# Optimization experiments

Hardware: AMD Instinct MI355X
Metric: run time of the kernel (lower is better)

## Reference

```python
import jax, jax.numpy as jnp
import numpy as np

NUM_HEADS = 8
NUM_GROUPS = 32  # min(C//4, 32) for C=512
EPS = 1e-6       # flax GroupNorm default


def setup_inputs() -> dict:
    key = jax.random.key(0)
    ks = jax.random.split(key, 3)
    B, H, W, D, C = 2, 16, 16, 16, 512
    x = jax.random.normal(ks[0], (B, H, W, D, C), dtype=jnp.float32)
    w_qkv = jax.random.normal(ks[1], (C, 3 * C), dtype=jnp.float32) / np.sqrt(C)
    w_proj = jax.random.normal(ks[2], (C, C), dtype=jnp.float32) / np.sqrt(C)
    return {
        "x": x,
        "gn_scale": jnp.ones((C,), jnp.float32),
        "gn_bias": jnp.zeros((C,), jnp.float32),
        "w_qkv": w_qkv,
        "b_qkv": jnp.zeros((3 * C,), jnp.float32),
        "w_proj": w_proj,
        "b_proj": jnp.zeros((C,), jnp.float32),
    }


def group_norm(x, scale, bias):
    # x: [B, S, C]; normalize within each of NUM_GROUPS channel groups over (S, group-channels)
    B, S, C = x.shape
    xg = x.reshape(B, S, NUM_GROUPS, C // NUM_GROUPS)
    mean = jnp.mean(xg, axis=(1, 3), keepdims=True)
    var = jnp.var(xg, axis=(1, 3), keepdims=True)
    xn = (xg - mean) * jax.lax.rsqrt(var + EPS)
    return xn.reshape(B, S, C) * scale + bias


def reference(x, gn_scale, gn_bias, w_qkv, b_qkv, w_proj, b_proj):
    B, H, W, D, C = x.shape
    S = H * W * D
    hd = C // NUM_HEADS
    xf = x.reshape(B, S, C)
    q_in = group_norm(xf, gn_scale, gn_bias)
    # 1x1x1 conv == per-position dense
    qkv = q_in @ w_qkv + b_qkv                      # [B, S, 3C]
    qkv = qkv.reshape(B, S, NUM_HEADS, 3 * hd)
    q, k, v = jnp.split(qkv, 3, axis=-1)            # each [B, S, nh, hd]
    scale = 1.0 / jnp.sqrt(jnp.asarray(hd, x.dtype))
    logits = jnp.einsum('btnh,bfnh->bnft', k, q * scale)  # [B, nh, S, S]
    weights = jax.nn.softmax(logits, axis=-1)
    h = jnp.einsum('bnft,btnh->bfnh', weights, v)   # [B, S, nh, hd]
    h = h.reshape(B, S, C) @ w_proj + b_proj
    return h.reshape(x.shape) + x
```

## Files before the change

kernel.cpp:

```cpp
#include <hip/hip_runtime.h>

typedef __attribute__((ext_vector_type(8))) short short8;
typedef __attribute__((ext_vector_type(4))) float f32x4;
typedef __attribute__((ext_vector_type(16))) float f32x16;

#define S_LEN 4096
#define C_DIM 512
#define NH 8
#define HD 64
#define NG 32
#define GS 16
#define LOG2E 1.44269504088896340736f

__device__ __forceinline__ unsigned short f2bf(float f) {
  union { float f; unsigned int u; } v; v.f = f;
  unsigned int r = v.u + 0x7fffu + ((v.u >> 16) & 1u);
  return (unsigned short)(r >> 16);
}

__device__ __forceinline__ float bf2f(unsigned short s) {
  union { unsigned u; float f; } v; v.u = (unsigned)s << 16;
  return v.f;
}

__device__ __forceinline__ float fexp2(float x) {
  float r;
  asm("v_exp_f32 %0, %1" : "=v"(r) : "v"(x));
  return r;
}

__device__ __forceinline__ unsigned pk_bf16(float a, float b) {
  unsigned r;
  asm("v_cvt_pk_bf16_f32 %0, %1, %2" : "=v"(r) : "v"(a), "v"(b));
  return r;
}

__device__ __forceinline__ void pl_swap(unsigned& a, unsigned& b) {
  asm("v_permlane32_swap_b32 %0, %1" : "+v"(a), "+v"(b));
}
__device__ __forceinline__ void pl_swapf(float& a, float& b) {
  asm("v_permlane32_swap_b32 %0, %1" : "+v"(a), "+v"(b));
}

__device__ __forceinline__ void gload_lds16(const void* g, void* l) {
  __builtin_amdgcn_global_load_lds((const __attribute__((address_space(1))) void*)g,
                                   (__attribute__((address_space(3))) void*)l, 16, 0, 0);
}

__global__ __launch_bounds__(256) void prep_kernel(const float* __restrict__ x,
                                                   float* __restrict__ partials,
                                                   const float* __restrict__ w_qkv,
                                                   unsigned short* __restrict__ wqkvT,
                                                   const float* __restrict__ w_proj,
                                                   unsigned short* __restrict__ wprojT) {
  __shared__ float tile[32][33];
  __shared__ float r1[4], r2[4];
  int bid = blockIdx.x;
  if (bid < 256) {
    int bg = bid >> 2, chunk = bid & 3;
    int b = bg >> 5, g = bg & 31;
    const float* xp = x + (size_t)b * S_LEN * C_DIM + g * GS;
    float s1 = 0.f, s2 = 0.f;
    for (int i = threadIdx.x; i < 1024 * 4; i += 256) {
      int s = chunk * 1024 + (i >> 2), c4 = i & 3;
      float4 v = *(const float4*)&xp[(size_t)s * C_DIM + c4 * 4];
      s1 += v.x + v.y + v.z + v.w;
      s2 += v.x * v.x + v.y * v.y + v.z * v.z + v.w * v.w;
    }
    for (int off = 1; off < 64; off <<= 1) {
      s1 += __shfl_xor(s1, off);
      s2 += __shfl_xor(s2, off);
    }
    int w = threadIdx.x >> 6;
    if ((threadIdx.x & 63) == 0) { r1[w] = s1; r2[w] = s2; }
    __syncthreads();
    if (threadIdx.x == 0) {
      partials[bg * 8 + chunk * 2]     = r1[0] + r1[1] + r1[2] + r1[3];
      partials[bg * 8 + chunk * 2 + 1] = r2[0] + r2[1] + r2[2] + r2[3];
    }
    return;
  }
  const float* src; unsigned short* dst; int K, N, n0, k0;
  if (bid < 1024) {
    int t = bid - 256;  src = w_qkv;  dst = wqkvT;  K = 512; N = 1536;
    n0 = (t % 48) * 32; k0 = (t / 48) * 32;
  } else {
    int t = bid - 1024; src = w_proj; dst = wprojT; K = 512; N = 512;
    n0 = (t % 16) * 32; k0 = (t / 16) * 32;
  }
  int c = threadIdx.x & 31, r0 = threadIdx.x >> 5;
  for (int i = 0; i < 4; ++i) {
    int r = r0 + i * 8;
    tile[r][c] = src[(size_t)(k0 + r) * N + n0 + c];
  }
  __syncthreads();
  for (int i = 0; i < 4; ++i) {
    int r = r0 + i * 8;
    dst[(size_t)(n0 + r) * K + k0 + c] = f2bf(tile[c][r]);
  }
}

__global__ __launch_bounds__(256) void gemm_qkv_kernel(const float* __restrict__ x,
                                                       const float* __restrict__ partials,
                                                       const float* __restrict__ gscale,
                                                       const float* __restrict__ gbias,
                                                       const unsigned short* __restrict__ Bt,
                                                       const float* __restrict__ qbias,
                                                       unsigned short* __restrict__ qh,
                                                       unsigned short* __restrict__ kh,
                                                       unsigned short* __restrict__ vh) {
  __shared__ unsigned char Alds[16384];
  __shared__ unsigned char Blds[16384];
  __shared__ float AsL[512], CsL[512];
  int tid = threadIdx.x, lane = tid & 63, w = tid >> 6;
  int li = lane & 15, g = lane >> 4;
  int wr = (w >> 1) * 64, wc = (w & 1) * 64;
  int m0 = blockIdx.y * 128, n0 = blockIdx.x * 128;
  int b_ = m0 >> 12;

  int srow = tid >> 3;
  int colS = (tid & 7) * 16;
  int sc   = colS ^ ((srow & 7) << 4);
  const char* bSrc = (const char*)Bt + (size_t)(n0 + srow) * 1024 + sc;

  const float invN = 1.0f / (float)(S_LEN * GS);
#pragma unroll
  for (int i = 0; i < 2; ++i) {
    int c = tid + i * 256;
    int bg = b_ * NG + (c >> 4);
    float s1 = partials[bg * 8] + partials[bg * 8 + 2] + partials[bg * 8 + 4] + partials[bg * 8 + 6];
    float s2 = partials[bg * 8 + 1] + partials[bg * 8 + 3] + partials[bg * 8 + 5] + partials[bg * 8 + 7];
    float mean = s1 * invN;
    float var = s2 * invN - mean * mean;
    float rstd = rsqrtf(var + 1e-6f);
    float A_ = rstd * gscale[c];
    AsL[c] = A_;
    CsL[c] = gbias[c] - mean * A_;
  }
  __syncthreads();

  int tr = tid >> 1, hf2 = tid & 1;
  const float* xRow = x + (size_t)(m0 + tr) * C_DIM + hf2 * 32;

  f32x4 acc[4][4];
  for (int i = 0; i < 4; ++i)
    for (int j = 0; j < 4; ++j) acc[i][j] = (f32x4){0.f, 0.f, 0.f, 0.f};

  for (int k0 = 0; k0 < 512; k0 += 64) {
    float4 xv[8];
#pragma unroll
    for (int q = 0; q < 8; ++q) xv[q] = *(const float4*)&xRow[k0 + q * 4];
#pragma unroll
    for (int r = 0; r < 4; ++r)
      gload_lds16(bSrc + (size_t)r * 32 * 1024 + k0 * 2, &Blds[r * 4096 + tid * 16]);

    int cbase = k0 + hf2 * 32;
#pragma unroll
    for (int q = 0; q < 4; ++q) {
      union { unsigned u[4]; short8 v; } d;
#pragma unroll
      for (int p = 0; p < 2; ++p) {
        int c = cbase + q * 8 + p * 4;
        float4 A4 = *(const float4*)&AsL[c];
        float4 C4 = *(const float4*)&CsL[c];
        float4 vv = xv[2 * q + p];
        d.u[p * 2]     = pk_bf16(vv.x * A4.x + C4.x, vv.y * A4.y + C4.y);
        d.u[p * 2 + 1] = pk_bf16(vv.z * A4.z + C4.z, vv.w * A4.w + C4.w);
      }
      int cc = hf2 * 64 + q * 16;
      *(short8*)&Alds[tr * 128 + (cc ^ ((tr & 7) << 4))] = d.v;
    }
    __syncthreads();

#pragma unroll
    for (int ks = 0; ks < 2; ++ks) {
      short8 af[4], bfm[4];
#pragma unroll
      for (int mi = 0; mi < 4; ++mi) {
        int row = wr + mi * 16 + li;
        af[mi] = *(const short8*)&Alds[row * 128 + ((ks * 64 + g * 16) ^ ((row & 7) << 4))];
      }
#pragma unroll
      for (int ni = 0; ni < 4; ++ni) {
        int row = wc + ni * 16 + li;
        bfm[ni] = *(const short8*)&Blds[row * 128 + ((ks * 64 + g * 16) ^ ((row & 7) << 4))];
      }
#pragma unroll
      for (int mi = 0; mi < 4; ++mi)
#pragma unroll
        for (int ni = 0; ni < 4; ++ni)
          acc[mi][ni] = __builtin_amdgcn_mfma_f32_16x16x32_bf16(af[mi], bfm[ni], acc[mi][ni], 0, 0, 0);
    }
    __syncthreads();
  }

  for (int ni = 0; ni < 4; ++ni) {
    int n = n0 + wc + ni * 16 + li;
    float bn = qbias[n];
    int head = n / 192;
    int rem = n - head * 192;
    int part = rem >> 6;
    int h = rem & 63;
    if (part == 2) {
      for (int mi = 0; mi < 4; ++mi) {
        int m = m0 + wr + mi * 16 + g * 4;
        int b = m >> 12, s = m & 4095;
        size_t idx = ((size_t)(b * NH + head) * HD + h) * S_LEN + s;
        ushort4 val;
        val.x = f2bf(acc[mi][ni][0] + bn);
        val.y = f2bf(acc[mi][ni][1] + bn);
        val.z = f2bf(acc[mi][ni][2] + bn);
        val.w = f2bf(acc[mi][ni][3] + bn);
        *(ushort4*)&vh[idx] = val;
      }
    } else {
      unsigned short* dst = part == 0 ? qh : kh;
      float mul = part == 0 ? 0.125f * LOG2E : 1.0f;
      for (int mi = 0; mi < 4; ++mi)
        for (int j = 0; j < 4; ++j) {
          int m = m0 + wr + mi * 16 + g * 4 + j;
          int b = m >> 12, s = m & 4095;
          dst[((size_t)(b * NH + head) * S_LEN + s) * HD + h] = f2bf((acc[mi][ni][j] + bn) * mul);
        }
    }
  }
}

__global__ __launch_bounds__(256) void gemm_plain_kernel(const unsigned short* __restrict__ A,
                                                         const unsigned short* __restrict__ Bt,
                                                         const float* __restrict__ bias,
                                                         const float* __restrict__ resid,
                                                         float* __restrict__ outf) {
  __shared__ unsigned char Alds[16384];
  __shared__ unsigned char Blds[16384];
  int tid = threadIdx.x, lane = tid & 63, w = tid >> 6;
  int li = lane & 15, g = lane >> 4;
  int wr = (w >> 1) * 64, wc = (w & 1) * 64;
  int m0 = blockIdx.y * 128, n0 = blockIdx.x * 128;

  int srow = tid >> 3;
  int colS = (tid & 7) * 16;
  int sc   = colS ^ ((srow & 7) << 4);
  const char* aSrc = (const char*)A + (size_t)(m0 + srow) * 1024 + sc;
  const char* bSrc = (const char*)Bt + (size_t)(n0 + srow) * 1024 + sc;

  f32x4 acc[4][4];
  for (int i = 0; i < 4; ++i)
    for (int j = 0; j < 4; ++j) acc[i][j] = (f32x4){0.f, 0.f, 0.f, 0.f};

  for (int k0 = 0; k0 < 512; k0 += 64) {
#pragma unroll
    for (int r = 0; r < 4; ++r) {
      gload_lds16(aSrc + (size_t)r * 32 * 1024 + k0 * 2, &Alds[r * 4096 + tid * 16]);
      gload_lds16(bSrc + (size_t)r * 32 * 1024 + k0 * 2, &Blds[r * 4096 + tid * 16]);
    }
    asm volatile("s_waitcnt vmcnt(0)" ::: "memory");
    __builtin_amdgcn_s_barrier();
#pragma unroll
    for (int ks = 0; ks < 2; ++ks) {
      short8 af[4], bfm[4];
#pragma unroll
      for (int mi = 0; mi < 4; ++mi) {
        int row = wr + mi * 16 + li;
        af[mi] = *(const short8*)&Alds[row * 128 + ((ks * 64 + g * 16) ^ ((row & 7) << 4))];
      }
#pragma unroll
      for (int ni = 0; ni < 4; ++ni) {
        int row = wc + ni * 16 + li;
        bfm[ni] = *(const short8*)&Blds[row * 128 + ((ks * 64 + g * 16) ^ ((row & 7) << 4))];
      }
#pragma unroll
      for (int mi = 0; mi < 4; ++mi)
#pragma unroll
        for (int ni = 0; ni < 4; ++ni)
          acc[mi][ni] = __builtin_amdgcn_mfma_f32_16x16x32_bf16(af[mi], bfm[ni], acc[mi][ni], 0, 0, 0);
    }
    __syncthreads();
  }

  for (int ni = 0; ni < 4; ++ni) {
    int n = n0 + wc + ni * 16 + li;
    float bn = bias[n];
    for (int mi = 0; mi < 4; ++mi)
      for (int j = 0; j < 4; ++j) {
        int m = m0 + wr + mi * 16 + g * 4 + j;
        size_t off = (size_t)m * C_DIM + n;
        outf[off] = acc[mi][ni][j] + bn + resid[off];
      }
  }
}

__global__ __launch_bounds__(256) void gemm_proj_kernel(const unsigned short* __restrict__ opart,
                                                        const float* __restrict__ lpart,
                                                        const unsigned short* __restrict__ Bt,
                                                        const float* __restrict__ bias,
                                                        const float* __restrict__ resid,
                                                        float* __restrict__ outf) {
  __shared__ unsigned char Alds[16384];
  __shared__ unsigned char Blds[16384];
  __shared__ float linv[8][128];
  int tid = threadIdx.x, lane = tid & 63, w = tid >> 6;
  int li = lane & 15, g = lane >> 4;
  int wr = (w >> 1) * 64, wc = (w & 1) * 64;
  int m0 = blockIdx.y * 128, n0 = blockIdx.x * 128;
  int b_ = m0 >> 12;
  int s0 = m0 & 4095;

  int srow = tid >> 3;
  int colS = (tid & 7) * 16;
  int sc   = colS ^ ((srow & 7) << 4);
  const char* bSrc = (const char*)Bt + (size_t)(n0 + srow) * 1024 + sc;

#pragma unroll
  for (int i = 0; i < 4; ++i) {
    int e = tid + i * 256;
    int hd_ = e >> 7, r = e & 127;
    size_t rowA = (size_t)((b_ * NH + hd_) * 2) * S_LEN + s0 + r;
    linv[hd_][r] = 1.0f / (lpart[rowA] + lpart[rowA + S_LEN]);
  }
  __syncthreads();

  int tr = tid >> 1, hf2 = tid & 1;
  size_t rowBase = ((size_t)(b_ * NH) * 2) * S_LEN + s0 + tr;

  f32x4 acc[4][4];
  for (int i = 0; i < 4; ++i)
    for (int j = 0; j < 4; ++j) acc[i][j] = (f32x4){0.f, 0.f, 0.f, 0.f};

  for (int k0 = 0; k0 < 512; k0 += 64) {
    int head = k0 >> 6;
#pragma unroll
    for (int r = 0; r < 4; ++r)
      gload_lds16(bSrc + (size_t)r * 32 * 1024 + k0 * 2, &Blds[r * 4096 + tid * 16]);

    size_t rowA = rowBase + (size_t)head * 2 * S_LEN;
    const unsigned short* pA0 = opart + rowA * 64 + hf2 * 32;
    const unsigned short* pA1 = opart + (rowA + S_LEN) * 64 + hf2 * 32;
    float inv = linv[head][tr];
#pragma unroll
    for (int q = 0; q < 4; ++q) {
      short8 xx = *(const short8*)&pA0[q * 8];
      short8 yy = *(const short8*)&pA1[q * 8];
      union { unsigned u[4]; short8 v; } d;
#pragma unroll
      for (int p = 0; p < 4; ++p) {
        float f0 = (bf2f((unsigned short)xx[2 * p])     + bf2f((unsigned short)yy[2 * p]))     * inv;
        float f1 = (bf2f((unsigned short)xx[2 * p + 1]) + bf2f((unsigned short)yy[2 * p + 1])) * inv;
        d.u[p] = pk_bf16(f0, f1);
      }
      int cc = hf2 * 64 + q * 16;
      *(short8*)&Alds[tr * 128 + (cc ^ ((tr & 7) << 4))] = d.v;
    }
    __syncthreads();

#pragma unroll
    for (int ks = 0; ks < 2; ++ks) {
      short8 af[4], bfm[4];
#pragma unroll
      for (int mi = 0; mi < 4; ++mi) {
        int row = wr + mi * 16 + li;
        af[mi] = *(const short8*)&Alds[row * 128 + ((ks * 64 + g * 16) ^ ((row & 7) << 4))];
      }
#pragma unroll
      for (int ni = 0; ni < 4; ++ni) {
        int row = wc + ni * 16 + li;
        bfm[ni] = *(const short8*)&Blds[row * 128 + ((ks * 64 + g * 16) ^ ((row & 7) << 4))];
      }
#pragma unroll
      for (int mi = 0; mi < 4; ++mi)
#pragma unroll
        for (int ni = 0; ni < 4; ++ni)
          acc[mi][ni] = __builtin_amdgcn_mfma_f32_16x16x32_bf16(af[mi], bfm[ni], acc[mi][ni], 0, 0, 0);
    }
    __syncthreads();
  }

  for (int ni = 0; ni < 4; ++ni) {
    int n = n0 + wc + ni * 16 + li;
    float bn = bias[n];
    for (int mi = 0; mi < 4; ++mi)
      for (int j = 0; j < 4; ++j) {
        int m = m0 + wr + mi * 16 + g * 4 + j;
        size_t off = (size_t)m * C_DIM + n;
        outf[off] = acc[mi][ni][j] + bn + resid[off];
      }
  }
}

template <int SPLIT>
__global__ __launch_bounds__(256, 4) void attn_kernel(const unsigned short* __restrict__ qh,
                                                      const unsigned short* __restrict__ kh,
                                                      const unsigned short* __restrict__ vt,
                                                      unsigned short* __restrict__ ob,
                                                      unsigned short* __restrict__ opart,
                                                      float* __restrict__ lpart) {
  __shared__ unsigned char Kt[3 * 4096];
  __shared__ unsigned char Vt[3 * 4096];
  int bn = blockIdx.y;
  int half = SPLIT > 1 ? blockIdx.z : 0;
  int tid = threadIdx.x, lane = tid & 63, wv = tid >> 6;
  int r32 = lane & 31, hi_ = lane >> 5;
  int q0 = blockIdx.x * 128 + wv * 32;
  const int NT = S_LEN / 32 / SPLIT;
  const unsigned short* qp = qh + (size_t)bn * S_LEN * HD;
  const char* kp = (const char*)(kh + (size_t)bn * S_LEN * HD);
  const char* vp = (const char*)(vt + (size_t)bn * HD * S_LEN);

  int srow  = wv * 8 + (lane >> 3);
  int scolS = (lane & 7) * 16;
  int sc    = scolS ^ ((srow & 7) << 4);
  const char* kSrc = kp + (size_t)srow * 128 + sc + (size_t)half * (S_LEN / SPLIT) * 128;
  int vh_ = srow + ((sc >> 6) << 5);
  const char* vSrc = vp + (size_t)vh_ * (S_LEN * 2) + (sc & 63) + (size_t)half * (S_LEN / SPLIT) * 2;

  short8 qf[4];
#pragma unroll
  for (int ks = 0; ks < 4; ++ks)
    qf[ks] = *(const short8*)&qp[(size_t)(q0 + r32) * HD + ks * 16 + hi_ * 8];

  f32x16 o0, o1, z16;
#pragma unroll
  for (int i = 0; i < 16; ++i) { o0[i] = 0.f; o1[i] = 0.f; z16[i] = 0.f; }
  float lsum = 0.f;

  int swzr = (r32 & 7) << 4;
  int sBase = wv * 1024;

  gload_lds16(kSrc, &Kt[sBase]);
  gload_lds16(vSrc, &Vt[sBase]);
  gload_lds16(kSrc + 32 * 128, &Kt[4096 + sBase]);
  gload_lds16(vSrc + 32 * 2,   &Vt[4096 + sBase]);
  asm volatile("s_waitcnt vmcnt(2)" ::: "memory");
  __builtin_amdgcn_s_barrier();

  int curO = 0, nxtO = 4096, nnO = 8192;
  for (int it = 0; it < NT; ++it) {
    bool more = (it + 2 < NT);
    if (more) {
      size_t t0n = (size_t)(it + 2) * 32;
      gload_lds16(kSrc + t0n * 128, &Kt[nnO + sBase]);
      gload_lds16(vSrc + t0n * 2,   &Vt[nnO + sBase]);
    }

    const unsigned char* Kr = &Kt[curO + r32 * 128];
    const unsigned char* Vr = &Vt[curO + r32 * 128];
    short8 kf[4], vf[4];
#pragma unroll
    for (int ks = 0; ks < 4; ++ks)
      kf[ks] = *(const short8*)&Kr[(ks * 32 + hi_ * 16) ^ swzr];
#pragma unroll
    for (int kk = 0; kk < 2; ++kk)
#pragma unroll
      for (int hf = 0; hf < 2; ++hf)
        vf[kk * 2 + hf] = *(const short8*)&Vr[(hf * 64 + kk * 32 + hi_ * 16) ^ swzr];

    f32x16 s = __builtin_amdgcn_mfma_f32_32x32x16_bf16(kf[0], qf[0], z16, 0, 0, 0);
#pragma unroll
    for (int ks = 1; ks < 4; ++ks)
      s = __builtin_amdgcn_mfma_f32_32x32x16_bf16(kf[ks], qf[ks], s, 0, 0, 0);

#pragma unroll
    for (int i = 0; i < 16; ++i) s[i] = fexp2(s[i]);

    float t0 = (s[0] + s[1]) + (s[2] + s[3]);
    float t1 = (s[4] + s[5]) + (s[6] + s[7]);
    float t2 = (s[8] + s[9]) + (s[10] + s[11]);
    float t3 = (s[12] + s[13]) + (s[14] + s[15]);
    lsum += (t0 + t1) + (t2 + t3);

    unsigned pkv[8];
#pragma unroll
    for (int g2 = 0; g2 < 8; ++g2) pkv[g2] = pk_bf16(s[2 * g2], s[2 * g2 + 1]);
    pl_swap(pkv[0], pkv[2]); pl_swap(pkv[1], pkv[3]);
    pl_swap(pkv[4], pkv[6]); pl_swap(pkv[5], pkv[7]);
    union { unsigned u[4]; short8 v; } F0, F1;
    F0.u[0] = pkv[0]; F0.u[1] = pkv[1]; F0.u[2] = pkv[2]; F0.u[3] = pkv[3];
    F1.u[0] = pkv[4]; F1.u[1] = pkv[5]; F1.u[2] = pkv[6]; F1.u[3] = pkv[7];

    o0 = __builtin_amdgcn_mfma_f32_32x32x16_bf16(vf[0], F0.v, o0, 0, 0, 0);
    o1 = __builtin_amdgcn_mfma_f32_32x32x16_bf16(vf[1], F0.v, o1, 0, 0, 0);
    o0 = __builtin_amdgcn_mfma_f32_32x32x16_bf16(vf[2], F1.v, o0, 0, 0, 0);
    o1 = __builtin_amdgcn_mfma_f32_32x32x16_bf16(vf[3], F1.v, o1, 0, 0, 0);

    if (more) asm volatile("s_waitcnt vmcnt(2)" ::: "memory");
    else      asm volatile("s_waitcnt vmcnt(0)" ::: "memory");
    __builtin_amdgcn_s_barrier();
    int t = curO; curO = nxtO; nxtO = nnO; nnO = t;
  }

  { float c2 = lsum; pl_swapf(lsum, c2); lsum += c2; }

  if (SPLIT == 1) {
    float inv = 1.0f / lsum;
    int b = bn >> 3, n = bn & 7;
    size_t base = ((size_t)(b * S_LEN + q0 + r32)) * C_DIM + n * HD;
#pragma unroll
    for (int r = 0; r < 16; ++r) {
      int hrow = (r & 3) + 8 * (r >> 2) + 4 * hi_;
      ob[base + hrow]      = f2bf(o0[r] * inv);
      ob[base + 32 + hrow] = f2bf(o1[r] * inv);
    }
  } else {
    size_t row = (size_t)(bn * SPLIT + half) * S_LEN + q0 + r32;
    unsigned short* pp = opart + row * 64;
#pragma unroll
    for (int i = 0; i < 8; ++i) {
      int r = 2 * i;
      int hrow = (r & 3) + 8 * (r >> 2) + 4 * hi_;
      *(unsigned*)&pp[hrow]      = pk_bf16(o0[r], o0[r + 1]);
      *(unsigned*)&pp[32 + hrow] = pk_bf16(o1[r], o1[r + 1]);
    }
    if (!hi_) lpart[row] = lsum;
  }
}

extern "C" void kernel_launch(void* const* d_in, const int* in_sizes, int n_in,
                              void* d_out, int out_size, void* d_ws, size_t ws_size,
                              hipStream_t stream) {
  const float* x        = (const float*)d_in[0];
  const float* gn_scale = (const float*)d_in[1];
  const float* gn_bias  = (const float*)d_in[2];
  const float* w_qkv    = (const float*)d_in[3];
  const float* b_qkv    = (const float*)d_in[4];
  const float* w_proj   = (const float*)d_in[5];
  const float* b_proj   = (const float*)d_in[6];
  float* out = (float*)d_out;

  char* ws = (char*)d_ws;
  unsigned short* wqkvT  = (unsigned short*)(ws + 8388608);
  unsigned short* wprojT = (unsigned short*)(ws + 9961472);
  unsigned short* qhb    = (unsigned short*)(ws + 10485760);
  unsigned short* khb    = (unsigned short*)(ws + 18874368);
  unsigned short* vtb    = (unsigned short*)(ws + 27262976);
  unsigned short* ahb    = (unsigned short*)(ws + 35651584);
  float* partials        = (float*)(ws + 44040192);
  float* lpart           = (float*)(ws + 44042240);
  unsigned short* opart  = (unsigned short*)(ws + 45090816);
  const size_t NEED2 = 45090816ull + (size_t)16 * 2 * S_LEN * 64 * 2;

  prep_kernel<<<1280, 256, 0, stream>>>(x, partials, w_qkv, wqkvT, w_proj, wprojT);
  gemm_qkv_kernel<<<dim3(12, 64), 256, 0, stream>>>(x, partials, gn_scale, gn_bias, wqkvT, b_qkv,
                                                    qhb, khb, vtb);
  if (ws_size >= NEED2) {
    attn_kernel<2><<<dim3(32, 16, 2), 256, 0, stream>>>(qhb, khb, vtb, nullptr, opart, lpart);
    gemm_proj_kernel<<<dim3(4, 64), 256, 0, stream>>>(opart, lpart, wprojT, b_proj, x, out);
  } else {
    attn_kernel<1><<<dim3(32, 16, 1), 256, 0, stream>>>(qhb, khb, vtb, ahb, nullptr, nullptr);
    gemm_plain_kernel<<<dim3(4, 64), 256, 0, stream>>>(ahb, wprojT, b_proj, x, out);
  }
}
```

Measured before the change: 164.5 us.

## Split GroupNorm apply into separate bf16 pass before QKV GEMM

GroupNorm application moves out of the QKV GEMM prologue into a standalone kernel that writes normalized bf16 activations to workspace. The GEMM then loads both A and B tiles with direct global-to-LDS loads, dropping the per-block stats recompute, the fp32 x reads and the per-tile conversion work. The cost is an extra kernel launch and an extra round trip through memory for the 8MB normalized activation (read 16MB fp32, write 8MB bf16). The GEMM also loads x once instead of 12 times, since each of the 12 column blocks previously reread it.

Measured after the change: 147.5 us. 1.12x faster.

```diff
diff --git a/kernel.cpp b/kernel.cpp
--- a/kernel.cpp
+++ b/kernel.cpp
@@ -100,77 +100,63 @@
   }
 }
 
-__global__ __launch_bounds__(256) void gemm_qkv_kernel(const float* __restrict__ x,
+__global__ __launch_bounds__(256) void gn_apply_kernel(const float* __restrict__ x,
                                                        const float* __restrict__ partials,
-                                                       const float* __restrict__ gscale,
-                                                       const float* __restrict__ gbias,
+                                                       const float* __restrict__ scale,
+                                                       const float* __restrict__ bias,
+                                                       unsigned short* __restrict__ out) {
+  int idx = blockIdx.x * 256 + threadIdx.x;
+  int e = idx * 4;
+  int c = e & (C_DIM - 1);
+  int bs = e >> 9;
+  int b = bs >> 12;
+  int grp = b * NG + (c >> 4);
+  float s1 = partials[grp * 8] + partials[grp * 8 + 2] + partials[grp * 8 + 4] + partials[grp * 8 + 6];
+  float s2 = partials[grp * 8 + 1] + partials[grp * 8 + 3] + partials[grp * 8 + 5] + partials[grp * 8 + 7];
+  const float invN = 1.0f / (float)(S_LEN * GS);
+  float mean = s1 * invN;
+  float var = s2 * invN - mean * mean;
+  float rstd = rsqrtf(var + 1e-6f);
+  float4 v = *(const float4*)&x[e];
+  ushort4 o;
+  o.x = f2bf((v.x - mean) * rstd * scale[c]     + bias[c]);
+  o.y = f2bf((v.y - mean) * rstd * scale[c + 1] + bias[c + 1]);
+  o.z = f2bf((v.z - mean) * rstd * scale[c + 2] + bias[c + 2]);
+  o.w = f2bf((v.w - mean) * rstd * scale[c + 3] + bias[c + 3]);
+  *(ushort4*)&out[e] = o;
+}
+
+__global__ __launch_bounds__(256) void gemm_qkv_kernel(const unsigned short* __restrict__ A,
                                                        const unsigned short* __restrict__ Bt,
-                                                       const float* __restrict__ qbias,
+                                                       const float* __restrict__ bias,
                                                        unsigned short* __restrict__ qh,
                                                        unsigned short* __restrict__ kh,
                                                        unsigned short* __restrict__ vh) {
   __shared__ unsigned char Alds[16384];
   __shared__ unsigned char Blds[16384];
-  __shared__ float AsL[512], CsL[512];
   int tid = threadIdx.x, lane = tid & 63, w = tid >> 6;
   int li = lane & 15, g = lane >> 4;
   int wr = (w >> 1) * 64, wc = (w & 1) * 64;
   int m0 = blockIdx.y * 128, n0 = blockIdx.x * 128;
-  int b_ = m0 >> 12;
 
   int srow = tid >> 3;
   int colS = (tid & 7) * 16;
   int sc   = colS ^ ((srow & 7) << 4);
+  const char* aSrc = (const char*)A + (size_t)(m0 + srow) * 1024 + sc;
   const char* bSrc = (const char*)Bt + (size_t)(n0 + srow) * 1024 + sc;
-
-  const float invN = 1.0f / (float)(S_LEN * GS);
-#pragma unroll
-  for (int i = 0; i < 2; ++i) {
-    int c = tid + i * 256;
-    int bg = b_ * NG + (c >> 4);
-    float s1 = partials[bg * 8] + partials[bg * 8 + 2] + partials[bg * 8 + 4] + partials[bg * 8 + 6];
-    float s2 = partials[bg * 8 + 1] + partials[bg * 8 + 3] + partials[bg * 8 + 5] + partials[bg * 8 + 7];
-    float mean = s1 * invN;
-    float var = s2 * invN - mean * mean;
-    float rstd = rsqrtf(var + 1e-6f);
-    float A_ = rstd * gscale[c];
-    AsL[c] = A_;
-    CsL[c] = gbias[c] - mean * A_;
-  }
-  __syncthreads();
-
-  int tr = tid >> 1, hf2 = tid & 1;
-  const float* xRow = x + (size_t)(m0 + tr) * C_DIM + hf2 * 32;
 
   f32x4 acc[4][4];
   for (int i = 0; i < 4; ++i)
     for (int j = 0; j < 4; ++j) acc[i][j] = (f32x4){0.f, 0.f, 0.f, 0.f};
 
   for (int k0 = 0; k0 < 512; k0 += 64) {
-    float4 xv[8];
-#pragma unroll
-    for (int q = 0; q < 8; ++q) xv[q] = *(const float4*)&xRow[k0 + q * 4];
-#pragma unroll
-    for (int r = 0; r < 4; ++r)
+#pragma unroll
+    for (int r = 0; r < 4; ++r) {
+      gload_lds16(aSrc + (size_t)r * 32 * 1024 + k0 * 2, &Alds[r * 4096 + tid * 16]);
       gload_lds16(bSrc + (size_t)r * 32 * 1024 + k0 * 2, &Blds[r * 4096 + tid * 16]);
-
-    int cbase = k0 + hf2 * 32;
-#pragma unroll
-    for (int q = 0; q < 4; ++q) {
-      union { unsigned u[4]; short8 v; } d;
-#pragma unroll
-      for (int p = 0; p < 2; ++p) {
-        int c = cbase + q * 8 + p * 4;
-        float4 A4 = *(const float4*)&AsL[c];
-        float4 C4 = *(const float4*)&CsL[c];
-        float4 vv = xv[2 * q + p];
-        d.u[p * 2]     = pk_bf16(vv.x * A4.x + C4.x, vv.y * A4.y + C4.y);
-        d.u[p * 2 + 1] = pk_bf16(vv.z * A4.z + C4.z, vv.w * A4.w + C4.w);
-      }
-      int cc = hf2 * 64 + q * 16;
-      *(short8*)&Alds[tr * 128 + (cc ^ ((tr & 7) << 4))] = d.v;
-    }
-    __syncthreads();
+    }
+    asm volatile("s_waitcnt vmcnt(0)" ::: "memory");
+    __builtin_amdgcn_s_barrier();
 
 #pragma unroll
     for (int ks = 0; ks < 2; ++ks) {
@@ -196,7 +182,7 @@
 
   for (int ni = 0; ni < 4; ++ni) {
     int n = n0 + wc + ni * 16 + li;
-    float bn = qbias[n];
+    float bn = bias[n];
     int head = n / 192;
     int rem = n - head * 192;
     int part = rem >> 6;
@@ -527,6 +513,7 @@
   float* out = (float*)d_out;
 
   char* ws = (char*)d_ws;
+  unsigned short* q_in   = (unsigned short*)(ws);
   unsigned short* wqkvT  = (unsigned short*)(ws + 8388608);
   unsigned short* wprojT = (unsigned short*)(ws + 9961472);
   unsigned short* qhb    = (unsigned short*)(ws + 10485760);
@@ -539,8 +526,8 @@
   const size_t NEED2 = 45090816ull + (size_t)16 * 2 * S_LEN * 64 * 2;
 
   prep_kernel<<<1280, 256, 0, stream>>>(x, partials, w_qkv, wqkvT, w_proj, wprojT);
-  gemm_qkv_kernel<<<dim3(12, 64), 256, 0, stream>>>(x, partials, gn_scale, gn_bias, wqkvT, b_qkv,
-                                                    qhb, khb, vtb);
+  gn_apply_kernel<<<4096, 256, 0, stream>>>(x, partials, gn_scale, gn_bias, q_in);
+  gemm_qkv_kernel<<<dim3(12, 64), 256, 0, stream>>>(q_in, wqkvT, b_qkv, qhb, khb, vtb);
   if (ws_size >= NEED2) {
     attn_kernel<2><<<dim3(32, 16, 2), 256, 0, stream>>>(qhb, khb, vtb, nullptr, opart, lpart);
     gemm_proj_kernel<<<dim3(4, 64), 256, 0, stream>>>(opart, lpart, wprojT, b_proj, x, out);
```
